# Kernel optimization log

Hardware: AMD Instinct MI355X
Metric: run time of the kernel (lower is better)

Reference implementation:

```python
import jax, jax.numpy as jnp
import numpy as np

EPS = 1e-12  # torch F.normalize eps


def setup_inputs() -> dict:
    key = jax.random.key(0)
    k1, k2, k3 = jax.random.split(key, 3)
    N, C, H, W, K = 32, 128, 112, 112, 64
    x = jax.random.normal(k1, (N, C, H, W), dtype=jnp.float32)
    conv_w = jax.random.normal(k2, (K, C), dtype=jnp.float32) * 0.05  # 1x1 conv weight, no bias (vladv2=False)
    centroids = jax.random.uniform(k3, (K, C), dtype=jnp.float32)
    return {"x": x, "conv_w": conv_w, "centroids": centroids}


def reference(x, conv_w, centroids):
    N, C = x.shape[:2]
    K = centroids.shape[0]
    xf = x.reshape(N, C, -1)                       # (N, C, S)
    # 1x1 conv == per-pixel linear: (K,C) @ (N,C,S) -> (N,K,S)
    soft_assign = jnp.einsum('kc,ncs->nks', conv_w, xf)
    soft_assign = jax.nn.softmax(soft_assign, axis=1)  # softmax over clusters
    # vlad[n,k,c] = sum_s a[n,k,s] * (x[n,c,s] - cent[k,c])
    vlad = jnp.einsum('nks,ncs->nkc', soft_assign, xf) \
         - soft_assign.sum(axis=-1)[..., None] * centroids[None, :, :]
    # intra-normalize over descriptor dim
    vlad = vlad / jnp.maximum(jnp.linalg.norm(vlad, axis=2, keepdims=True), EPS)
    vlad = vlad.reshape(N, K * C)
    vlad = vlad / jnp.maximum(jnp.linalg.norm(vlad, axis=1, keepdims=True), EPS)
    return vlad
```

## Files before the change

kernel.cpp:

```cpp
#include <hip/hip_runtime.h>
#include <hip/hip_bf16.h>

#define NV_N 32
#define NV_C 128
#define NV_K 64
#define NV_S 12544
#define ST 64
#define TILES 14
#define SCHUNK 14
#define AS 72

typedef short short8 __attribute__((ext_vector_type(8)));
typedef float floatx4 __attribute__((ext_vector_type(4)));

static __device__ __forceinline__ unsigned short f2bf(float f) {
  union { float f; unsigned u; } v; v.f = f;
  unsigned r = v.u + 0x7FFFu + ((v.u >> 16) & 1u);
  return (unsigned short)(r >> 16);
}
static __device__ __forceinline__ unsigned pk2(float a, float b) {
  union { __hip_bfloat162 h; unsigned u; } v;
  v.h = __float22bfloat162_rn(make_float2(a, b));
  return v.u;
}
static __device__ __forceinline__ short8 pack8(float4 a, float4 b) {
  union { unsigned u[4]; short8 s; } r;
  r.u[0] = pk2(a.x, a.y); r.u[1] = pk2(a.z, a.w);
  r.u[2] = pk2(b.x, b.y); r.u[3] = pk2(b.z, b.w);
  return r.s;
}
static __device__ __forceinline__ short8 pack8s(const float* f) {
  union { unsigned u[4]; short8 s; } r;
  r.u[0] = pk2(f[0], f[1]); r.u[1] = pk2(f[2], f[3]);
  r.u[2] = pk2(f[4], f[5]); r.u[3] = pk2(f[6], f[7]);
  return r.s;
}

__global__ __launch_bounds__(256, 2) void netvlad_main(
    const float* __restrict__ x, const float* __restrict__ conv_w,
    float* __restrict__ vlad_ws, float* __restrict__ asum_ws) {
  __shared__ __attribute__((aligned(16))) unsigned short a_lds[2][NV_K * AS];
  __shared__ float asum_sh[4][NV_K];

  const int t = threadIdx.x;
  const int n = blockIdx.x / SCHUNK;
  const int chunk = blockIdx.x % SCHUNK;
  const int s_base = chunk * (ST * TILES);
  const int w = t >> 6;
  const int lane = t & 63;
  const int q = lane >> 4;
  const int l = lane & 15;

  const float* __restrict__ xn = x + (size_t)n * NV_C * NV_S;

  short8 wfrag[4][4];
#pragma unroll
  for (int mt = 0; mt < 4; ++mt)
#pragma unroll
    for (int kc = 0; kc < 4; ++kc) {
      const float* wp = conv_w + (mt * 16 + l) * NV_C + kc * 32 + q * 8;
      wfrag[mt][kc] = pack8(*(const float4*)wp, *(const float4*)(wp + 4));
    }

  floatx4 acc2[4][2];
  float asum_acc[4][4];
#pragma unroll
  for (int mt = 0; mt < 4; ++mt) {
#pragma unroll
    for (int nt = 0; nt < 2; ++nt) acc2[mt][nt] = (floatx4){0.f, 0.f, 0.f, 0.f};
#pragma unroll
    for (int r = 0; r < 4; ++r) asum_acc[mt][r] = 0.f;
  }

  const float* __restrict__ xg1 = xn + (size_t)(q * 8) * NV_S + s_base + w * 16 + l;
  const float* __restrict__ xg2a = xn + (size_t)((w * 2 + 0) * 16 + l) * NV_S + s_base + q * 8;
  const float* __restrict__ xg2b = xn + (size_t)((w * 2 + 1) * 16 + l) * NV_S + s_base + q * 8;

  for (int tt = 0; tt < TILES; ++tt) {
    const int buf = tt & 1;
    const int so = tt * ST;

    float bxf[4][8];
#pragma unroll
    for (int kc = 0; kc < 4; ++kc)
#pragma unroll
      for (int j = 0; j < 8; ++j)
        bxf[kc][j] = xg1[(size_t)(kc * 32 + j) * NV_S + so];

    float4 p2[2][2][2];
#pragma unroll
    for (int sk = 0; sk < 2; ++sk) {
      p2[0][sk][0] = *(const float4*)(xg2a + so + sk * 32);
      p2[0][sk][1] = *(const float4*)(xg2a + so + sk * 32 + 4);
      p2[1][sk][0] = *(const float4*)(xg2b + so + sk * 32);
      p2[1][sk][1] = *(const float4*)(xg2b + so + sk * 32 + 4);
    }

    floatx4 acc1[4];
#pragma unroll
    for (int mt = 0; mt < 4; ++mt) acc1[mt] = (floatx4){0.f, 0.f, 0.f, 0.f};
#pragma unroll
    for (int kc = 0; kc < 4; ++kc) {
      const short8 bfr = pack8s(bxf[kc]);
#pragma unroll
      for (int mt = 0; mt < 4; ++mt)
        acc1[mt] = __builtin_amdgcn_mfma_f32_16x16x32_bf16(wfrag[mt][kc], bfr, acc1[mt], 0, 0, 0);
    }

    {
      float sum = 0.f;
#pragma unroll
      for (int mt = 0; mt < 4; ++mt)
#pragma unroll
        for (int r = 0; r < 4; ++r) {
          float e = __expf(acc1[mt][r]);
          acc1[mt][r] = e; sum += e;
        }
      sum += __shfl_xor(sum, 16);
      sum += __shfl_xor(sum, 32);
      const float inv = 1.0f / sum;
#pragma unroll
      for (int mt = 0; mt < 4; ++mt)
#pragma unroll
        for (int r = 0; r < 4; ++r) {
          float a = acc1[mt][r] * inv;
          asum_acc[mt][r] += a;
          a_lds[buf][(mt * 16 + q * 4 + r) * AS + w * 16 + l] = f2bf(a);
        }
    }
    __syncthreads();

#pragma unroll
    for (int sk = 0; sk < 2; ++sk) {
      short8 afr[4];
#pragma unroll
      for (int mt = 0; mt < 4; ++mt)
        afr[mt] = *(const short8*)&a_lds[buf][(mt * 16 + l) * AS + sk * 32 + q * 8];
#pragma unroll
      for (int nt = 0; nt < 2; ++nt) {
        const short8 bfr = pack8(p2[nt][sk][0], p2[nt][sk][1]);
#pragma unroll
        for (int mt = 0; mt < 4; ++mt)
          acc2[mt][nt] = __builtin_amdgcn_mfma_f32_16x16x32_bf16(afr[mt], bfr, acc2[mt][nt], 0, 0, 0);
      }
    }
  }

#pragma unroll
  for (int mt = 0; mt < 4; ++mt)
#pragma unroll
    for (int r = 0; r < 4; ++r) {
      float v = asum_acc[mt][r];
      v += __shfl_xor(v, 1); v += __shfl_xor(v, 2);
      v += __shfl_xor(v, 4); v += __shfl_xor(v, 8);
      if (l == 0) asum_sh[w][mt * 16 + q * 4 + r] = v;
    }
  __syncthreads();
  const size_t slab = (size_t)(n * SCHUNK + chunk);
  if (t < NV_K)
    asum_ws[slab * NV_K + t] =
        asum_sh[0][t] + asum_sh[1][t] + asum_sh[2][t] + asum_sh[3][t];

  float* vw = vlad_ws + slab * (NV_K * NV_C);
#pragma unroll
  for (int mt = 0; mt < 4; ++mt)
#pragma unroll
    for (int nt = 0; nt < 2; ++nt)
#pragma unroll
      for (int r = 0; r < 4; ++r)
        vw[(mt * 16 + q * 4 + r) * NV_C + (w * 2 + nt) * 16 + l] = acc2[mt][nt][r];
}

__global__ __launch_bounds__(256) void netvlad_reduce(
    const float* __restrict__ vlad_ws, const float* __restrict__ asum_ws,
    const float* __restrict__ cent, float* __restrict__ vlad_f) {
  const int t = threadIdx.x;
  const int n = blockIdx.x >> 3;
  const int k = (blockIdx.x & 7) * 8 + (t >> 5);
  const int c4 = (t & 31) * 4;

  float as = 0.f;
  float4 acc = {0.f, 0.f, 0.f, 0.f};
#pragma unroll
  for (int ch = 0; ch < SCHUNK; ++ch) {
    const size_t slab = (size_t)(n * SCHUNK + ch);
    as += asum_ws[slab * NV_K + k];
    float4 p = *(const float4*)&vlad_ws[slab * (NV_K * NV_C) + k * NV_C + c4];
    acc.x += p.x; acc.y += p.y; acc.z += p.z; acc.w += p.w;
  }
  float4 ce = *(const float4*)&cent[k * NV_C + c4];
  float4 v;
  v.x = acc.x - as * ce.x; v.y = acc.y - as * ce.y;
  v.z = acc.z - as * ce.z; v.w = acc.w - as * ce.w;
  *(float4*)&vlad_f[(size_t)n * (NV_K * NV_C) + k * NV_C + c4] = v;
}

__global__ __launch_bounds__(256) void netvlad_finalize(
    const float* __restrict__ vlad_f, float* __restrict__ out) {
  __shared__ float v_lds[NV_K * NV_C];
  __shared__ float red4[256];
  __shared__ float rscale[NV_K];
  __shared__ float gscale_sh;

  const int t = threadIdx.x; const int n = blockIdx.x;
  const float* vf = vlad_f + (size_t)n * (NV_K * NV_C);

#pragma unroll
  for (int i = 0; i < 8; ++i) {
    int vec = t + i * 256; int k = vec >> 5; int cq = vec & 31;
    *(float4*)&v_lds[k * NV_C + cq * 4] = *(const float4*)(vf + k * NV_C + cq * 4);
  }
  __syncthreads();

  {
    const int k = t >> 2, part = t & 3;
    const float* row = &v_lds[k * NV_C + part * 32];
    float ss = 0.0f;
#pragma unroll
    for (int c = 0; c < 32; ++c) { float v = row[c]; ss += v * v; }
    red4[t] = ss;
  }
  __syncthreads();
  if (t < NV_K) {
    float ss = red4[t * 4] + red4[t * 4 + 1] + red4[t * 4 + 2] + red4[t * 4 + 3];
    rscale[t] = 1.0f / fmaxf(sqrtf(ss), 1e-12f);
  }
  __syncthreads();

  float gp = 0.0f;
#pragma unroll
  for (int i = 0; i < 8; ++i) {
    int vec = t + i * 256; int k = vec >> 5; int cq = vec & 31;
    float4 v = *(const float4*)&v_lds[k * NV_C + cq * 4];
    float rs = rscale[k];
    gp += (v.x * v.x + v.y * v.y + v.z * v.z + v.w * v.w) * rs * rs;
  }
  red4[t] = gp;
  __syncthreads();
  if (t < 64) {
    float s = red4[t] + red4[t + 64] + red4[t + 128] + red4[t + 192];
#pragma unroll
    for (int o = 32; o > 0; o >>= 1) s += __shfl_down(s, o);
    if (t == 0) gscale_sh = 1.0f / fmaxf(sqrtf(s), 1e-12f);
  }
  __syncthreads();
  const float gs = gscale_sh;

#pragma unroll
  for (int i = 0; i < 8; ++i) {
    int vec = t + i * 256; int k = vec >> 5; int cq = vec & 31;
    float4 v = *(const float4*)&v_lds[k * NV_C + cq * 4];
    const float sc = rscale[k] * gs;
    v.x *= sc; v.y *= sc; v.z *= sc; v.w *= sc;
    *(float4*)(out + (size_t)n * (NV_K * NV_C) + k * NV_C + cq * 4) = v;
  }
}

extern "C" void kernel_launch(void* const* d_in, const int* in_sizes, int n_in,
                              void* d_out, int out_size, void* d_ws, size_t ws_size,
                              hipStream_t stream) {
  (void)in_sizes; (void)n_in; (void)out_size; (void)ws_size;
  const float* x      = (const float*)d_in[0];
  const float* conv_w = (const float*)d_in[1];
  const float* cent   = (const float*)d_in[2];
  float* out = (float*)d_out;

  float* vlad_ws = (float*)d_ws;
  float* asum_ws = vlad_ws + (size_t)NV_N * SCHUNK * NV_K * NV_C;
  float* vlad_f  = asum_ws + (size_t)NV_N * SCHUNK * NV_K;

  hipLaunchKernelGGL(netvlad_main, dim3(NV_N * SCHUNK), dim3(256), 0, stream,
                     x, conv_w, vlad_ws, asum_ws);
  hipLaunchKernelGGL(netvlad_reduce, dim3(NV_N * 8), dim3(256), 0, stream,
                     vlad_ws, asum_ws, cent, vlad_f);
  hipLaunchKernelGGL(netvlad_finalize, dim3(NV_N), dim3(256), 0, stream,
                     vlad_f, out);
}
```

Baseline: 309.9 us.

## Double grid size, split softmax across warps, fuse reduce and finalize kernels

The spatial chunk count goes from 14 to 28, so 896 blocks are launched, and launch bounds allow 4 blocks per CU for more occupancy and latency hiding on this memory-bound kernel. Each warp now computes half the clusters for two spatial subtiles, which halves the conv-weight fragment registers. The softmax denominator is combined across warps through LDS, costing an extra barrier per tile. The separate reduce and finalize kernels are merged into one per-batch tail kernel, dropping the intermediate vlad_f buffer and one launch, but the tail runs only 32 blocks that each read twice as many partial slabs.

```diff
diff --git a/kernel.cpp b/kernel.cpp
--- a/kernel.cpp
+++ b/kernel.cpp
@@ -6,8 +6,8 @@
 #define NV_K 64
 #define NV_S 12544
 #define ST 64
-#define TILES 14
-#define SCHUNK 14
+#define TILES 7
+#define SCHUNK 28
 #define AS 72
 
 typedef short short8 __attribute__((ext_vector_type(8)));
@@ -36,11 +36,12 @@
   return r.s;
 }
 
-__global__ __launch_bounds__(256, 2) void netvlad_main(
+__global__ __launch_bounds__(256, 4) void netvlad_main(
     const float* __restrict__ x, const float* __restrict__ conv_w,
     float* __restrict__ vlad_ws, float* __restrict__ asum_ws) {
   __shared__ __attribute__((aligned(16))) unsigned short a_lds[2][NV_K * AS];
-  __shared__ float asum_sh[4][NV_K];
+  __shared__ float sum_lds[2][2][ST];
+  __shared__ float asum_sh[4][32];
 
   const int t = threadIdx.x;
   const int n = blockIdx.x / SCHUNK;
@@ -50,29 +51,33 @@
   const int lane = t & 63;
   const int q = lane >> 4;
   const int l = lane & 15;
+  const int kh = w >> 1;
+  const int sp = w & 1;
 
   const float* __restrict__ xn = x + (size_t)n * NV_C * NV_S;
 
-  short8 wfrag[4][4];
+  short8 wfrag[2][4];
+#pragma unroll
+  for (int mt2 = 0; mt2 < 2; ++mt2)
+#pragma unroll
+    for (int kc = 0; kc < 4; ++kc) {
+      const float* wp = conv_w + (kh * 32 + mt2 * 16 + l) * NV_C + kc * 32 + q * 8;
+      wfrag[mt2][kc] = pack8(*(const float4*)wp, *(const float4*)(wp + 4));
+    }
+
+  floatx4 acc2[4][2];
+  float asum8[2][4];
 #pragma unroll
   for (int mt = 0; mt < 4; ++mt)
 #pragma unroll
-    for (int kc = 0; kc < 4; ++kc) {
-      const float* wp = conv_w + (mt * 16 + l) * NV_C + kc * 32 + q * 8;
-      wfrag[mt][kc] = pack8(*(const float4*)wp, *(const float4*)(wp + 4));
-    }
-
-  floatx4 acc2[4][2];
-  float asum_acc[4][4];
-#pragma unroll
-  for (int mt = 0; mt < 4; ++mt) {
-#pragma unroll
     for (int nt = 0; nt < 2; ++nt) acc2[mt][nt] = (floatx4){0.f, 0.f, 0.f, 0.f};
 #pragma unroll
-    for (int r = 0; r < 4; ++r) asum_acc[mt][r] = 0.f;
-  }
-
-  const float* __restrict__ xg1 = xn + (size_t)(q * 8) * NV_S + s_base + w * 16 + l;
+  for (int mt2 = 0; mt2 < 2; ++mt2)
+#pragma unroll
+    for (int r = 0; r < 4; ++r) asum8[mt2][r] = 0.f;
+
+  const float* __restrict__ xg1_0 = xn + (size_t)(q * 8) * NV_S + s_base + (2 * sp + 0) * 16 + l;
+  const float* __restrict__ xg1_1 = xg1_0 + 16;
   const float* __restrict__ xg2a = xn + (size_t)((w * 2 + 0) * 16 + l) * NV_S + s_base + q * 8;
   const float* __restrict__ xg2b = xn + (size_t)((w * 2 + 1) * 16 + l) * NV_S + s_base + q * 8;
 
@@ -80,52 +85,62 @@
     const int buf = tt & 1;
     const int so = tt * ST;
 
-    float bxf[4][8];
-#pragma unroll
-    for (int kc = 0; kc < 4; ++kc)
-#pragma unroll
-      for (int j = 0; j < 8; ++j)
-        bxf[kc][j] = xg1[(size_t)(kc * 32 + j) * NV_S + so];
-
-    float4 p2[2][2][2];
-#pragma unroll
-    for (int sk = 0; sk < 2; ++sk) {
-      p2[0][sk][0] = *(const float4*)(xg2a + so + sk * 32);
-      p2[0][sk][1] = *(const float4*)(xg2a + so + sk * 32 + 4);
-      p2[1][sk][0] = *(const float4*)(xg2b + so + sk * 32);
-      p2[1][sk][1] = *(const float4*)(xg2b + so + sk * 32 + 4);
-    }
-
-    floatx4 acc1[4];
-#pragma unroll
-    for (int mt = 0; mt < 4; ++mt) acc1[mt] = (floatx4){0.f, 0.f, 0.f, 0.f};
-#pragma unroll
-    for (int kc = 0; kc < 4; ++kc) {
-      const short8 bfr = pack8s(bxf[kc]);
-#pragma unroll
-      for (int mt = 0; mt < 4; ++mt)
-        acc1[mt] = __builtin_amdgcn_mfma_f32_16x16x32_bf16(wfrag[mt][kc], bfr, acc1[mt], 0, 0, 0);
+    floatx4 acc1[2][2];
+#pragma unroll
+    for (int mt2 = 0; mt2 < 2; ++mt2)
+#pragma unroll
+      for (int st2 = 0; st2 < 2; ++st2) acc1[mt2][st2] = (floatx4){0.f, 0.f, 0.f, 0.f};
+
+#pragma unroll
+    for (int st2 = 0; st2 < 2; ++st2) {
+      const float* __restrict__ xb = st2 ? xg1_1 : xg1_0;
+#pragma unroll
+      for (int kc = 0; kc < 4; ++kc) {
+        float bx[8];
+#pragma unroll
+        for (int j = 0; j < 8; ++j)
+          bx[j] = xb[(size_t)(kc * 32 + j) * NV_S + so];
+        const short8 bfr = pack8s(bx);
+#pragma unroll
+        for (int mt2 = 0; mt2 < 2; ++mt2)
+          acc1[mt2][st2] = __builtin_amdgcn_mfma_f32_16x16x32_bf16(wfrag[mt2][kc], bfr, acc1[mt2][st2], 0, 0, 0);
+      }
     }
 
     {
-      float sum = 0.f;
-#pragma unroll
-      for (int mt = 0; mt < 4; ++mt)
+      float colp[2];
+#pragma unroll
+      for (int st2 = 0; st2 < 2; ++st2) {
+        float s = 0.f;
+#pragma unroll
+        for (int mt2 = 0; mt2 < 2; ++mt2)
+#pragma unroll
+          for (int r = 0; r < 4; ++r) {
+            float e = __expf(acc1[mt2][st2][r]);
+            acc1[mt2][st2][r] = e; s += e;
+          }
+        s += __shfl_xor(s, 16);
+        s += __shfl_xor(s, 32);
+        colp[st2] = s;
+      }
+      if (q == 0) {
+        sum_lds[buf][kh][(2 * sp + 0) * 16 + l] = colp[0];
+        sum_lds[buf][kh][(2 * sp + 1) * 16 + l] = colp[1];
+      }
+    }
+    __syncthreads();
+
+#pragma unroll
+    for (int st2 = 0; st2 < 2; ++st2) {
+      const int si = (2 * sp + st2) * 16 + l;
+      const float inv = 1.0f / (sum_lds[buf][0][si] + sum_lds[buf][1][si]);
+#pragma unroll
+      for (int mt2 = 0; mt2 < 2; ++mt2)
 #pragma unroll
         for (int r = 0; r < 4; ++r) {
-          float e = __expf(acc1[mt][r]);
-          acc1[mt][r] = e; sum += e;
-        }
-      sum += __shfl_xor(sum, 16);
-      sum += __shfl_xor(sum, 32);
-      const float inv = 1.0f / sum;
-#pragma unroll
-      for (int mt = 0; mt < 4; ++mt)
-#pragma unroll
-        for (int r = 0; r < 4; ++r) {
-          float a = acc1[mt][r] * inv;
-          asum_acc[mt][r] += a;
-          a_lds[buf][(mt * 16 + q * 4 + r) * AS + w * 16 + l] = f2bf(a);
+          float a = acc1[mt2][st2][r] * inv;
+          asum8[mt2][r] += a;
+          a_lds[buf][(kh * 32 + mt2 * 16 + q * 4 + r) * AS + si] = f2bf(a);
         }
     }
     __syncthreads();
@@ -136,30 +151,37 @@
 #pragma unroll
       for (int mt = 0; mt < 4; ++mt)
         afr[mt] = *(const short8*)&a_lds[buf][(mt * 16 + l) * AS + sk * 32 + q * 8];
-#pragma unroll
-      for (int nt = 0; nt < 2; ++nt) {
-        const short8 bfr = pack8(p2[nt][sk][0], p2[nt][sk][1]);
+      {
+        const short8 b0 = pack8(*(const float4*)(xg2a + so + sk * 32),
+                                *(const float4*)(xg2a + so + sk * 32 + 4));
 #pragma unroll
         for (int mt = 0; mt < 4; ++mt)
-          acc2[mt][nt] = __builtin_amdgcn_mfma_f32_16x16x32_bf16(afr[mt], bfr, acc2[mt][nt], 0, 0, 0);
-      }
-    }
-  }
-
-#pragma unroll
-  for (int mt = 0; mt < 4; ++mt)
+          acc2[mt][0] = __builtin_amdgcn_mfma_f32_16x16x32_bf16(afr[mt], b0, acc2[mt][0], 0, 0, 0);
+      }
+      {
+        const short8 b1 = pack8(*(const float4*)(xg2b + so + sk * 32),
+                                *(const float4*)(xg2b + so + sk * 32 + 4));
+#pragma unroll
+        for (int mt = 0; mt < 4; ++mt)
+          acc2[mt][1] = __builtin_amdgcn_mfma_f32_16x16x32_bf16(afr[mt], b1, acc2[mt][1], 0, 0, 0);
+      }
+    }
+  }
+
+#pragma unroll
+  for (int mt2 = 0; mt2 < 2; ++mt2)
 #pragma unroll
     for (int r = 0; r < 4; ++r) {
-      float v = asum_acc[mt][r];
+      float v = asum8[mt2][r];
       v += __shfl_xor(v, 1); v += __shfl_xor(v, 2);
       v += __shfl_xor(v, 4); v += __shfl_xor(v, 8);
-      if (l == 0) asum_sh[w][mt * 16 + q * 4 + r] = v;
+      if (l == 0) asum_sh[w][mt2 * 16 + q * 4 + r] = v;
     }
   __syncthreads();
   const size_t slab = (size_t)(n * SCHUNK + chunk);
   if (t < NV_K)
     asum_ws[slab * NV_K + t] =
-        asum_sh[0][t] + asum_sh[1][t] + asum_sh[2][t] + asum_sh[3][t];
+        asum_sh[2 * (t >> 5)][t & 31] + asum_sh[2 * (t >> 5) + 1][t & 31];
 
   float* vw = vlad_ws + slab * (NV_K * NV_C);
 #pragma unroll
@@ -171,74 +193,71 @@
         vw[(mt * 16 + q * 4 + r) * NV_C + (w * 2 + nt) * 16 + l] = acc2[mt][nt][r];
 }
 
-__global__ __launch_bounds__(256) void netvlad_reduce(
+__global__ __launch_bounds__(256) void netvlad_tail(
     const float* __restrict__ vlad_ws, const float* __restrict__ asum_ws,
-    const float* __restrict__ cent, float* __restrict__ vlad_f) {
-  const int t = threadIdx.x;
-  const int n = blockIdx.x >> 3;
-  const int k = (blockIdx.x & 7) * 8 + (t >> 5);
-  const int c4 = (t & 31) * 4;
-
-  float as = 0.f;
-  float4 acc = {0.f, 0.f, 0.f, 0.f};
-#pragma unroll
-  for (int ch = 0; ch < SCHUNK; ++ch) {
-    const size_t slab = (size_t)(n * SCHUNK + ch);
-    as += asum_ws[slab * NV_K + k];
-    float4 p = *(const float4*)&vlad_ws[slab * (NV_K * NV_C) + k * NV_C + c4];
-    acc.x += p.x; acc.y += p.y; acc.z += p.z; acc.w += p.w;
-  }
-  float4 ce = *(const float4*)&cent[k * NV_C + c4];
-  float4 v;
-  v.x = acc.x - as * ce.x; v.y = acc.y - as * ce.y;
-  v.z = acc.z - as * ce.z; v.w = acc.w - as * ce.w;
-  *(float4*)&vlad_f[(size_t)n * (NV_K * NV_C) + k * NV_C + c4] = v;
-}
-
-__global__ __launch_bounds__(256) void netvlad_finalize(
-    const float* __restrict__ vlad_f, float* __restrict__ out) {
-  __shared__ float v_lds[NV_K * NV_C];
-  __shared__ float red4[256];
+    const float* __restrict__ cent, float* __restrict__ out) {
+  __shared__ float asum_l[NV_K];
+  __shared__ float rowss[NV_K][33];
+  __shared__ float red[256];
   __shared__ float rscale[NV_K];
   __shared__ float gscale_sh;
 
   const int t = threadIdx.x; const int n = blockIdx.x;
-  const float* vf = vlad_f + (size_t)n * (NV_K * NV_C);
-
+  const int g = t >> 5;
+  const int c4 = (t & 31) * 4;
+
+  if (t < NV_K) {
+    float s = 0.f;
+#pragma unroll
+    for (int ch = 0; ch < SCHUNK; ++ch)
+      s += asum_ws[(size_t)(n * SCHUNK + ch) * NV_K + t];
+    asum_l[t] = s;
+  }
+
+  float4 acc[8];
+#pragma unroll
+  for (int i = 0; i < 8; ++i) acc[i] = (float4){0.f, 0.f, 0.f, 0.f};
+  for (int ch = 0; ch < SCHUNK; ++ch) {
+    const float* base = vlad_ws + (size_t)(n * SCHUNK + ch) * (NV_K * NV_C);
+#pragma unroll
+    for (int i = 0; i < 8; ++i) {
+      float4 p = *(const float4*)(base + i * 1024 + t * 4);
+      acc[i].x += p.x; acc[i].y += p.y; acc[i].z += p.z; acc[i].w += p.w;
+    }
+  }
+  __syncthreads();
+
+  float ss[8];
 #pragma unroll
   for (int i = 0; i < 8; ++i) {
-    int vec = t + i * 256; int k = vec >> 5; int cq = vec & 31;
-    *(float4*)&v_lds[k * NV_C + cq * 4] = *(const float4*)(vf + k * NV_C + cq * 4);
-  }
-  __syncthreads();
-
-  {
-    const int k = t >> 2, part = t & 3;
-    const float* row = &v_lds[k * NV_C + part * 32];
-    float ss = 0.0f;
-#pragma unroll
-    for (int c = 0; c < 32; ++c) { float v = row[c]; ss += v * v; }
-    red4[t] = ss;
+    const int k = i * 8 + g;
+    const float as = asum_l[k];
+    float4 ce = *(const float4*)&cent[k * NV_C + c4];
+    acc[i].x -= as * ce.x; acc[i].y -= as * ce.y;
+    acc[i].z -= as * ce.z; acc[i].w -= as * ce.w;
+    ss[i] = acc[i].x * acc[i].x + acc[i].y * acc[i].y +
+            acc[i].z * acc[i].z + acc[i].w * acc[i].w;
+    rowss[k][t & 31] = ss[i];
   }
   __syncthreads();
   if (t < NV_K) {
-    float ss = red4[t * 4] + red4[t * 4 + 1] + red4[t * 4 + 2] + red4[t * 4 + 3];
-    rscale[t] = 1.0f / fmaxf(sqrtf(ss), 1e-12f);
-  }
-  __syncthreads();
-
-  float gp = 0.0f;
+    float s = 0.f;
+#pragma unroll
+    for (int j = 0; j < 32; ++j) s += rowss[t][j];
+    rscale[t] = 1.0f / fmaxf(sqrtf(s), 1e-12f);
+  }
+  __syncthreads();
+
+  float gp = 0.f;
 #pragma unroll
   for (int i = 0; i < 8; ++i) {
-    int vec = t + i * 256; int k = vec >> 5; int cq = vec & 31;
-    float4 v = *(const float4*)&v_lds[k * NV_C + cq * 4];
-    float rs = rscale[k];
-    gp += (v.x * v.x + v.y * v.y + v.z * v.z + v.w * v.w) * rs * rs;
-  }
-  red4[t] = gp;
+    const float rs = rscale[i * 8 + g];
+    gp += ss[i] * rs * rs;
+  }
+  red[t] = gp;
   __syncthreads();
   if (t < 64) {
-    float s = red4[t] + red4[t + 64] + red4[t + 128] + red4[t + 192];
+    float s = red[t] + red[t + 64] + red[t + 128] + red[t + 192];
 #pragma unroll
     for (int o = 32; o > 0; o >>= 1) s += __shfl_down(s, o);
     if (t == 0) gscale_sh = 1.0f / fmaxf(sqrtf(s), 1e-12f);
@@ -248,11 +267,11 @@
 
 #pragma unroll
   for (int i = 0; i < 8; ++i) {
-    int vec = t + i * 256; int k = vec >> 5; int cq = vec & 31;
-    float4 v = *(const float4*)&v_lds[k * NV_C + cq * 4];
+    const int k = i * 8 + g;
     const float sc = rscale[k] * gs;
+    float4 v = acc[i];
     v.x *= sc; v.y *= sc; v.z *= sc; v.w *= sc;
-    *(float4*)(out + (size_t)n * (NV_K * NV_C) + k * NV_C + cq * 4) = v;
+    *(float4*)(out + (size_t)n * (NV_K * NV_C) + i * 1024 + t * 4) = v;
   }
 }
 
@@ -267,12 +286,9 @@
 
   float* vlad_ws = (float*)d_ws;
   float* asum_ws = vlad_ws + (size_t)NV_N * SCHUNK * NV_K * NV_C;
-  float* vlad_f  = asum_ws + (size_t)NV_N * SCHUNK * NV_K;
 
   hipLaunchKernelGGL(netvlad_main, dim3(NV_N * SCHUNK), dim3(256), 0, stream,
                      x, conv_w, vlad_ws, asum_ws);
-  hipLaunchKernelGGL(netvlad_reduce, dim3(NV_N * 8), dim3(256), 0, stream,
-                     vlad_ws, asum_ws, cent, vlad_f);
-  hipLaunchKernelGGL(netvlad_finalize, dim3(NV_N), dim3(256), 0, stream,
-                     vlad_f, out);
-}
+  hipLaunchKernelGGL(netvlad_tail, dim3(NV_N), dim3(256), 0, stream,
+                     vlad_ws, asum_ws, cent, out);
+}
```

Measured after the change: 366.6 us. 1.18x slower.
